# Performance work log

Hardware: AMD Instinct MI355X
Metric: run time of the kernel (lower is better)

Reference implementation:

```python
import jax, jax.numpy as jnp
import numpy as np

NUM_STATES = 128
TEMP = 1e-4


def setup_inputs() -> dict:
    key = jax.random.key(0)
    x = jax.random.uniform(key, (4, 8192, 8), dtype=jnp.float32)
    return {"x": x}


def reference(x):
    ns = NUM_STATES
    # normalize over time axis (dim=1)
    x_min = jnp.min(x, axis=1, keepdims=True)
    x_max = jnp.max(x, axis=1, keepdims=True)
    denom = jnp.maximum(x_max - x_min, 1e-8)
    xn = (x - x_min) / denom
    # StepDiscretizer (STE floor)
    scaled = jnp.clip(xn * (ns - 1), 0.0, ns - 1)
    hard_idx = jnp.floor(scaled)
    soft_index = jax.lax.stop_gradient(hard_idx - scaled) + scaled  # == floor numerically
    # (B, L, F) -> (B, F, L)
    idx = jnp.transpose(soft_index, (0, 2, 1))
    idx = jnp.clip(idx, 0.0, ns - 1)
    # soft one-hot: softmax of -(idx - states)^2 / temp over states
    states = jnp.arange(ns, dtype=jnp.float32)  # (ns,)
    logits = -((idx[..., None] - states) ** 2) / TEMP  # (B,F,L,ns)
    soft = jax.nn.softmax(logits, axis=-1)
    hard = jax.nn.one_hot(idx.astype(jnp.int32), ns, dtype=soft.dtype)
    S = jax.lax.stop_gradient(hard - soft) + soft  # (B,F,L,ns)
    # transition counts: S1^T @ S2 contracting time
    S1 = S[:, :, :-1, :]
    S2 = S[:, :, 1:, :]
    C = jnp.einsum('bfls,bflt->bfst', S1, S2)  # (B,F,ns,ns)
    row_sum = jnp.maximum(jnp.sum(C, axis=-1, keepdims=True), 1e-8)
    P = C / row_sum
    return P
```

## Files before the change

kernel.cpp:

```cpp
#include <hip/hip_runtime.h>


__device__ __forceinline__ float ieee_div_rn(float a, float d) {
    if (a == 0.0f) return 0.0f;
    unsigned ua = __float_as_uint(a), ud = __float_as_uint(d);
    int      Ea = (int)((ua >> 23) & 0xFFu);
    int      Ed = (int)((ud >> 23) & 0xFFu);
    unsigned Ma = ua & 0x7FFFFFu;
    unsigned Md = ud & 0x7FFFFFu;
    if (Ea) { Ma |= 0x800000u; } else { int sh = __clz(Ma) - 8; Ma <<= sh; Ea = 1 - sh; }
    if (Ed) { Md |= 0x800000u; } else { int sh = __clz(Md) - 8; Md <<= sh; Ed = 1 - sh; }
    unsigned long long num = (unsigned long long)Ma << 26;
    unsigned long long q0  = num / Md;
    unsigned long long rem = num - q0 * Md;
    unsigned Q, rnd; bool sticky; int Eout;
    if (q0 >= (1ull << 26)) {
        Q = (unsigned)(q0 >> 3); rnd = (unsigned)(q0 >> 2) & 1u;
        sticky = ((q0 & 3ull) != 0) || (rem != 0); Eout = Ea - Ed + 127;
    } else {
        Q = (unsigned)(q0 >> 2); rnd = (unsigned)(q0 >> 1) & 1u;
        sticky = ((q0 & 1ull) != 0) || (rem != 0); Eout = Ea - Ed + 126;
    }
    if (rnd && (sticky || (Q & 1u))) ++Q;
    if (Q == (1u << 24)) { Q = 1u << 23; ++Eout; }
    if (Eout < 1)   return 0.0f;
    if (Eout > 254) Eout = 254;
    return __uint_as_float(((unsigned)Eout << 23) | (Q & 0x7FFFFFu));
}

extern "C" __global__ __launch_bounds__(1024)
void MarkovTransition_50637664420500_kernel(const float* __restrict__ x,
                                            float* __restrict__ out)
{
    __shared__ unsigned int  cp[8192];
    __shared__ unsigned char bk0[1024];
    __shared__ float         rs[128];

    const int tid = threadIdx.x;
    const int bid = blockIdx.x;
    const float* xs = x + (bid >> 3) * 65536 + (bid & 7);

    float v[8];
    const int lbase = tid * 8;
    #pragma unroll
    for (int k = 0; k < 8; ++k) v[k] = xs[(lbase + k) * 8];

    float mn = v[0], mx = v[0];
    #pragma unroll
    for (int k = 1; k < 8; ++k) { mn = fminf(mn, v[k]); mx = fmaxf(mx, v[k]); }
    #pragma unroll
    for (int off = 32; off > 0; off >>= 1) {
        mn = fminf(mn, __shfl_xor(mn, off));
        mx = fmaxf(mx, __shfl_xor(mx, off));
    }
    const int wid = tid >> 6, lane = tid & 63;
    if (lane == 0) { cp[wid] = __float_as_uint(mn); cp[64 + wid] = __float_as_uint(mx); }
    __syncthreads();
    if (tid == 0) {
        float m0 = __uint_as_float(cp[0]), m1 = __uint_as_float(cp[64]);
        for (int t = 1; t < 16; ++t) {
            m0 = fminf(m0, __uint_as_float(cp[t]));
            m1 = fmaxf(m1, __uint_as_float(cp[64 + t]));
        }
        cp[128] = __float_as_uint(m0);
        cp[129] = __float_as_uint(m1);
    }
    __syncthreads();
    const float x_min = __uint_as_float(cp[128]);
    const float denom = fmaxf(__uint_as_float(cp[129]) - x_min, 1e-8f);
    const float inv   = ieee_div_rn(1.0f, denom);
    __syncthreads();

    int bk[8];
    #pragma unroll
    for (int k = 0; k < 8; ++k) {
        float a  = v[k] - x_min;
        float xn = a * inv;
        asm volatile("" : "+v"(xn));
        float s  = xn * 127.0f;
        s = fminf(fmaxf(s, 0.0f), 127.0f);
        bk[k] = (int)s;
    }
    bk0[tid] = (unsigned char)bk[0];
    #pragma unroll
    for (int i = 0; i < 8; ++i) cp[tid + i * 1024] = 0u;
    __syncthreads();

    #pragma unroll
    for (int k = 0; k < 7; ++k) {
        const int cell = bk[k] * 128 + bk[k + 1];
        atomicAdd(&cp[cell >> 1], 1u << ((cell & 1) << 4));
    }
    if (tid < 1023) {
        const int cell = bk[7] * 128 + (int)bk0[tid + 1];
        atomicAdd(&cp[cell >> 1], 1u << ((cell & 1) << 4));
    }
    __syncthreads();

    {
        const int j = tid & 7;
        unsigned s = 0;
        #pragma unroll
        for (int i = 0; i < 8; ++i) {
            const unsigned u = cp[tid * 8 + i];
            s += (u & 0xFFFFu) + (u >> 16);
        }
        s += __shfl_xor(s, 1);
        s += __shfl_xor(s, 2);
        s += __shfl_xor(s, 4);
        if (j == 0) rs[tid >> 3] = fmaxf((float)s, 1e-8f);
    }
    __syncthreads();

    float2* P2 = (float2*)(out + bid * 16384);
    #pragma unroll
    for (int i = 0; i < 8; ++i) {
        const int w = tid + i * 1024;
        const unsigned u = cp[w];
        const float r = rs[w >> 6];
        P2[w] = make_float2((float)(u & 0xFFFFu) / r, (float)(u >> 16) / r);
    }
}

extern "C" void kernel_launch(void* const* d_in, const int* in_sizes, int n_in,
                              void* d_out, int out_size, void* d_ws, size_t ws_size,
                              hipStream_t stream) {
    const float* x = (const float*)d_in[0];
    float* out = (float*)d_out;
    MarkovTransition_50637664420500_kernel<<<32, 1024, 0, stream>>>(x, out);
}
```

Baseline: 13.96 us.

## Split transition-count kernel into three launches using global workspace atomics

```diff
diff --git a/kernel.cpp b/kernel.cpp
--- a/kernel.cpp
+++ b/kernel.cpp
@@ -28,6 +28,130 @@
     return __uint_as_float(((unsigned)Eout << 23) | (Q & 0x7FFFFFu));
 }
 
+__device__ __forceinline__ int np_bucket(float v, float mn, float inv) {
+    float a  = v - mn;
+    float xn = a * inv;
+    asm volatile("" : "+v"(xn));
+    float s  = xn * 127.0f;
+    s = fminf(fmaxf(s, 0.0f), 127.0f);
+    return (int)s;
+}
+
+extern "C" __global__ __launch_bounds__(256)
+void mt_k1(const float* __restrict__ x, float* __restrict__ mnp,
+           float* __restrict__ mxp, unsigned int* __restrict__ cnt)
+{
+    __shared__ float smn[4][8], smx[4][8];
+    const int g = blockIdx.x, b = g >> 5, p = g & 31;
+    const int t = threadIdx.x;
+    const float* base = x + b * 65536 + (p * 256 + t) * 8;
+
+    float mn[8], mx[8];
+    #pragma unroll
+    for (int k = 0; k < 8; ++k) { float v = base[k]; mn[k] = v; mx[k] = v; }
+
+    unsigned int* cz = cnt + g * 4096;
+    #pragma unroll
+    for (int i = 0; i < 16; ++i) cz[t + i * 256] = 0u;
+
+    #pragma unroll
+    for (int off = 32; off > 0; off >>= 1) {
+        #pragma unroll
+        for (int k = 0; k < 8; ++k) {
+            mn[k] = fminf(mn[k], __shfl_xor(mn[k], off));
+            mx[k] = fmaxf(mx[k], __shfl_xor(mx[k], off));
+        }
+    }
+    const int wave = t >> 6, lane = t & 63;
+    if (lane == 0) {
+        #pragma unroll
+        for (int k = 0; k < 8; ++k) { smn[wave][k] = mn[k]; smx[wave][k] = mx[k]; }
+    }
+    __syncthreads();
+    if (t < 8) {
+        float a = smn[0][t], c = smx[0][t];
+        #pragma unroll
+        for (int w = 1; w < 4; ++w) { a = fminf(a, smn[w][t]); c = fmaxf(c, smx[w][t]); }
+        mnp[g * 8 + t] = a;
+        mxp[g * 8 + t] = c;
+    }
+}
+
+extern "C" __global__ __launch_bounds__(256)
+void mt_k2(const float* __restrict__ x, const float* __restrict__ mnp,
+           const float* __restrict__ mxp, unsigned int* __restrict__ cnt)
+{
+    __shared__ float s_mn[8], s_inv[8];
+    __shared__ unsigned char bkl[256 * 8];
+    const int g = blockIdx.x, b = g >> 5, p = g & 31;
+    const int t = threadIdx.x;
+    const int l = p * 256 + t;
+
+    if (t < 64) {
+        const int f = t & 7, q = t >> 3;
+        const int g0 = b * 32 + q * 4;
+        float a = mnp[g0 * 8 + f], c = mxp[g0 * 8 + f];
+        #pragma unroll
+        for (int i = 1; i < 4; ++i) {
+            a = fminf(a, mnp[(g0 + i) * 8 + f]);
+            c = fmaxf(c, mxp[(g0 + i) * 8 + f]);
+        }
+        a = fminf(a, __shfl_xor(a, 8));  c = fmaxf(c, __shfl_xor(c, 8));
+        a = fminf(a, __shfl_xor(a, 16)); c = fmaxf(c, __shfl_xor(c, 16));
+        a = fminf(a, __shfl_xor(a, 32)); c = fmaxf(c, __shfl_xor(c, 32));
+        if (t < 8) {
+            s_mn[t]  = a;
+            s_inv[t] = ieee_div_rn(1.0f, fmaxf(c - a, 1e-8f));
+        }
+    }
+    __syncthreads();
+
+    const float* base = x + b * 65536 + l * 8;
+    int bk[8];
+    #pragma unroll
+    for (int k = 0; k < 8; ++k) {
+        bk[k] = np_bucket(base[k], s_mn[k], s_inv[k]);
+        bkl[t * 8 + k] = (unsigned char)bk[k];
+    }
+    __syncthreads();
+
+    if (t < 255) {
+        #pragma unroll
+        for (int k = 0; k < 8; ++k) {
+            const int nb = (int)bkl[(t + 1) * 8 + k];
+            atomicAdd(&cnt[(b * 8 + k) * 16384 + bk[k] * 128 + nb], 1u);
+        }
+    } else if (l < 8191) {
+        const float* nx = x + b * 65536 + (l + 1) * 8;
+        #pragma unroll
+        for (int k = 0; k < 8; ++k) {
+            const int nb = np_bucket(nx[k], s_mn[k], s_inv[k]);
+            atomicAdd(&cnt[(b * 8 + k) * 16384 + bk[k] * 128 + nb], 1u);
+        }
+    }
+}
+
+extern "C" __global__ __launch_bounds__(256)
+void mt_k3(const unsigned int* __restrict__ cnt, float* __restrict__ out)
+{
+    const int g = blockIdx.x, s = g >> 3, rg = g & 7;
+    const int t = threadIdx.x;
+    const int row = rg * 16 + (t >> 4);
+    const int j = t & 15;
+    const unsigned int* c = cnt + s * 16384 + row * 128 + j * 8;
+    unsigned int u[8]; unsigned sum = 0;
+    #pragma unroll
+    for (int i = 0; i < 8; ++i) { u[i] = c[i]; sum += u[i]; }
+    sum += __shfl_xor(sum, 1);
+    sum += __shfl_xor(sum, 2);
+    sum += __shfl_xor(sum, 4);
+    sum += __shfl_xor(sum, 8);
+    const float rs = fmaxf((float)sum, 1e-8f);
+    float* o = out + s * 16384 + row * 128 + j * 8;
+    #pragma unroll
+    for (int i = 0; i < 8; ++i) o[i] = (float)u[i] / rs;
+}
+
 extern "C" __global__ __launch_bounds__(1024)
 void MarkovTransition_50637664420500_kernel(const float* __restrict__ x,
                                             float* __restrict__ out)
@@ -35,16 +159,12 @@
     __shared__ unsigned int  cp[8192];
     __shared__ unsigned char bk0[1024];
     __shared__ float         rs[128];
-
-    const int tid = threadIdx.x;
-    const int bid = blockIdx.x;
+    const int tid = threadIdx.x, bid = blockIdx.x;
     const float* xs = x + (bid >> 3) * 65536 + (bid & 7);
-
     float v[8];
     const int lbase = tid * 8;
     #pragma unroll
     for (int k = 0; k < 8; ++k) v[k] = xs[(lbase + k) * 8];
-
     float mn = v[0], mx = v[0];
     #pragma unroll
     for (int k = 1; k < 8; ++k) { mn = fminf(mn, v[k]); mx = fmaxf(mx, v[k]); }
@@ -58,34 +178,23 @@
     __syncthreads();
     if (tid == 0) {
         float m0 = __uint_as_float(cp[0]), m1 = __uint_as_float(cp[64]);
-        for (int t = 1; t < 16; ++t) {
-            m0 = fminf(m0, __uint_as_float(cp[t]));
-            m1 = fmaxf(m1, __uint_as_float(cp[64 + t]));
-        }
-        cp[128] = __float_as_uint(m0);
-        cp[129] = __float_as_uint(m1);
+        for (int t2 = 1; t2 < 16; ++t2) {
+            m0 = fminf(m0, __uint_as_float(cp[t2]));
+            m1 = fmaxf(m1, __uint_as_float(cp[64 + t2]));
+        }
+        cp[128] = __float_as_uint(m0); cp[129] = __float_as_uint(m1);
     }
     __syncthreads();
     const float x_min = __uint_as_float(cp[128]);
-    const float denom = fmaxf(__uint_as_float(cp[129]) - x_min, 1e-8f);
-    const float inv   = ieee_div_rn(1.0f, denom);
-    __syncthreads();
-
+    const float inv   = ieee_div_rn(1.0f, fmaxf(__uint_as_float(cp[129]) - x_min, 1e-8f));
+    __syncthreads();
     int bk[8];
     #pragma unroll
-    for (int k = 0; k < 8; ++k) {
-        float a  = v[k] - x_min;
-        float xn = a * inv;
-        asm volatile("" : "+v"(xn));
-        float s  = xn * 127.0f;
-        s = fminf(fmaxf(s, 0.0f), 127.0f);
-        bk[k] = (int)s;
-    }
+    for (int k = 0; k < 8; ++k) bk[k] = np_bucket(v[k], x_min, inv);
     bk0[tid] = (unsigned char)bk[0];
     #pragma unroll
     for (int i = 0; i < 8; ++i) cp[tid + i * 1024] = 0u;
     __syncthreads();
-
     #pragma unroll
     for (int k = 0; k < 7; ++k) {
         const int cell = bk[k] * 128 + bk[k + 1];
@@ -96,7 +205,6 @@
         atomicAdd(&cp[cell >> 1], 1u << ((cell & 1) << 4));
     }
     __syncthreads();
-
     {
         const int j = tid & 7;
         unsigned s = 0;
@@ -105,13 +213,10 @@
             const unsigned u = cp[tid * 8 + i];
             s += (u & 0xFFFFu) + (u >> 16);
         }
-        s += __shfl_xor(s, 1);
-        s += __shfl_xor(s, 2);
-        s += __shfl_xor(s, 4);
+        s += __shfl_xor(s, 1); s += __shfl_xor(s, 2); s += __shfl_xor(s, 4);
         if (j == 0) rs[tid >> 3] = fmaxf((float)s, 1e-8f);
     }
     __syncthreads();
-
     float2* P2 = (float2*)(out + bid * 16384);
     #pragma unroll
     for (int i = 0; i < 8; ++i) {
@@ -127,5 +232,15 @@
                               hipStream_t stream) {
     const float* x = (const float*)d_in[0];
     float* out = (float*)d_out;
-    MarkovTransition_50637664420500_kernel<<<32, 1024, 0, stream>>>(x, out);
-}
+    const size_t need = 8192 + (size_t)524288 * 4;
+    if (ws_size >= need) {
+        float* mnp = (float*)d_ws;
+        float* mxp = mnp + 1024;
+        unsigned int* cnt = (unsigned int*)((char*)d_ws + 8192);
+        mt_k1<<<128, 256, 0, stream>>>(x, mnp, mxp, cnt);
+        mt_k2<<<128, 256, 0, stream>>>(x, mnp, mxp, cnt);
+        mt_k3<<<256, 256, 0, stream>>>(cnt, out);
+    } else {
+        MarkovTransition_50637664420500_kernel<<<32, 1024, 0, stream>>>(x, out);
+    }
+}
```

New measurement: 26.20 us. 87.6% more time.

## Remap time indices per wave, shuffle-based transitions, float4 stores, block order swap

Applied to the files above, without the earlier changes.

```diff
diff --git a/kernel.cpp b/kernel.cpp
--- a/kernel.cpp
+++ b/kernel.cpp
@@ -28,22 +28,32 @@
     return __uint_as_float(((unsigned)Eout << 23) | (Q & 0x7FFFFFu));
 }
 
+__device__ __forceinline__ int np_bucket(float v, float mn, float inv) {
+    float a  = v - mn;
+    float xn = a * inv;
+    asm volatile("" : "+v"(xn));
+    float s  = xn * 127.0f;
+    s = fminf(fmaxf(s, 0.0f), 127.0f);
+    return (int)s;
+}
+
 extern "C" __global__ __launch_bounds__(1024)
 void MarkovTransition_50637664420500_kernel(const float* __restrict__ x,
                                             float* __restrict__ out)
 {
     __shared__ unsigned int  cp[8192];
-    __shared__ unsigned char bk0[1024];
+    __shared__ unsigned char wfirst[16];
     __shared__ float         rs[128];
 
-    const int tid = threadIdx.x;
-    const int bid = blockIdx.x;
-    const float* xs = x + (bid >> 3) * 65536 + (bid & 7);
+    const int tid  = threadIdx.x;
+    const int bid  = blockIdx.x;
+    const int b    = bid & 3, f = bid >> 2;
+    const int w    = tid >> 6, lane = tid & 63;
+    const float* xs = x + b * 65536 + f;
 
     float v[8];
-    const int lbase = tid * 8;
     #pragma unroll
-    for (int k = 0; k < 8; ++k) v[k] = xs[(lbase + k) * 8];
+    for (int k = 0; k < 8; ++k) v[k] = xs[(w * 512 + k * 64 + lane) * 8];
 
     float mn = v[0], mx = v[0];
     #pragma unroll
@@ -53,47 +63,42 @@
         mn = fminf(mn, __shfl_xor(mn, off));
         mx = fmaxf(mx, __shfl_xor(mx, off));
     }
-    const int wid = tid >> 6, lane = tid & 63;
-    if (lane == 0) { cp[wid] = __float_as_uint(mn); cp[64 + wid] = __float_as_uint(mx); }
+    if (lane == 0) { cp[w] = __float_as_uint(mn); cp[64 + w] = __float_as_uint(mx); }
     __syncthreads();
-    if (tid == 0) {
-        float m0 = __uint_as_float(cp[0]), m1 = __uint_as_float(cp[64]);
-        for (int t = 1; t < 16; ++t) {
-            m0 = fminf(m0, __uint_as_float(cp[t]));
-            m1 = fmaxf(m1, __uint_as_float(cp[64 + t]));
+    if (tid < 64) {
+        float m0 = (lane < 16) ? __uint_as_float(cp[lane])      :  3.0e38f;
+        float m1 = (lane < 16) ? __uint_as_float(cp[64 + lane]) : -3.0e38f;
+        #pragma unroll
+        for (int off = 8; off > 0; off >>= 1) {
+            m0 = fminf(m0, __shfl_xor(m0, off));
+            m1 = fmaxf(m1, __shfl_xor(m1, off));
         }
-        cp[128] = __float_as_uint(m0);
-        cp[129] = __float_as_uint(m1);
+        if (lane == 0) { cp[128] = __float_as_uint(m0); cp[129] = __float_as_uint(m1); }
     }
     __syncthreads();
     const float x_min = __uint_as_float(cp[128]);
-    const float denom = fmaxf(__uint_as_float(cp[129]) - x_min, 1e-8f);
-    const float inv   = ieee_div_rn(1.0f, denom);
+    const float inv   = ieee_div_rn(1.0f, fmaxf(__uint_as_float(cp[129]) - x_min, 1e-8f));
     __syncthreads();
 
     int bk[8];
     #pragma unroll
-    for (int k = 0; k < 8; ++k) {
-        float a  = v[k] - x_min;
-        float xn = a * inv;
-        asm volatile("" : "+v"(xn));
-        float s  = xn * 127.0f;
-        s = fminf(fmaxf(s, 0.0f), 127.0f);
-        bk[k] = (int)s;
-    }
-    bk0[tid] = (unsigned char)bk[0];
+    for (int k = 0; k < 8; ++k) bk[k] = np_bucket(v[k], x_min, inv);
+    if (lane == 0) wfirst[w] = (unsigned char)bk[0];
     #pragma unroll
     for (int i = 0; i < 8; ++i) cp[tid + i * 1024] = 0u;
     __syncthreads();
 
     #pragma unroll
-    for (int k = 0; k < 7; ++k) {
-        const int cell = bk[k] * 128 + bk[k + 1];
-        atomicAdd(&cp[cell >> 1], 1u << ((cell & 1) << 4));
-    }
-    if (tid < 1023) {
-        const int cell = bk[7] * 128 + (int)bk0[tid + 1];
-        atomicAdd(&cp[cell >> 1], 1u << ((cell & 1) << 4));
+    for (int k = 0; k < 8; ++k) {
+        int bc0;
+        if (k < 7) bc0 = __shfl(bk[k + 1], 0);
+        else       bc0 = (w < 15) ? (int)wfirst[w + 1] : -1;
+        int nb = __shfl_down(bk[k], 1);
+        if (lane == 63) nb = bc0;
+        if (nb >= 0) {
+            const int cell = bk[k] * 128 + nb;
+            atomicAdd(&cp[cell >> 1], 1u << ((cell & 1) << 4));
+        }
     }
     __syncthreads();
 
@@ -112,13 +117,15 @@
     }
     __syncthreads();
 
-    float2* P2 = (float2*)(out + bid * 16384);
+    float4* P4 = (float4*)(out + (b * 8 + f) * 16384);
     #pragma unroll
-    for (int i = 0; i < 8; ++i) {
-        const int w = tid + i * 1024;
-        const unsigned u = cp[w];
-        const float r = rs[w >> 6];
-        P2[w] = make_float2((float)(u & 0xFFFFu) / r, (float)(u >> 16) / r);
+    for (int i = 0; i < 4; ++i) {
+        const int idx = tid + i * 1024;
+        const unsigned u0 = cp[2 * idx];
+        const unsigned u1 = cp[2 * idx + 1];
+        const float r = rs[idx >> 5];
+        P4[idx] = make_float4((float)(u0 & 0xFFFFu) / r, (float)(u0 >> 16) / r,
+                              (float)(u1 & 0xFFFFu) / r, (float)(u1 >> 16) / r);
     }
 }
 
```

After: 14.41 us. 3.2% more time.
